# Optimization experiments

Hardware: AMD Instinct MI355X
Metric: run time of the kernel (lower is better)

## Reference

```python
import jax, jax.numpy as jnp
import numpy as np

B, T, D = 32, 4096, 256
W = 128          # window_size
EPS = 1e-5


def setup_inputs() -> dict:
    key = jax.random.key(0)
    kx, = jax.random.split(key, 1)
    x = jax.random.normal(kx, (B, T, D), dtype=jnp.float32)
    weight = jnp.ones((D,), dtype=jnp.float32)
    bias = jnp.zeros((D,), dtype=jnp.float32)
    return {"x": x, "weight": weight, "bias": bias}


def reference(x, weight, bias):
    # TemporalNorm, mode='standard', causal rolling window W, no mask, affine.
    Bs, Ts, Ds = x.shape
    idx = jnp.arange(Ts)
    l = jnp.clip(idx - W + 1, 0, None)   # left window index (inclusive)
    r = idx                               # right window index (inclusive, causal)

    # inclusive prefix sums over time, padded with a leading zero row
    sx = jnp.cumsum(x, axis=1)
    sx2 = jnp.cumsum(x * x, axis=1)

    def window_sum(cum):
        cum_pad = jnp.pad(cum, ((0, 0), (1, 0), (0, 0)))  # [B, T+1, D]
        return cum_pad[:, r + 1, :] - cum_pad[:, l, :]     # [B, T, D]

    win_sx = window_sum(sx)
    win_sx2 = window_sum(sx2)

    # mask is None -> per-window count = r - l + 1 (cumsum of ones)
    counts = (r - l + 1).astype(x.dtype)                   # [T]
    denom = jnp.maximum(counts, 1.0)[None, :, None]        # [1, T, 1]

    loc = win_sx / denom
    var = win_sx2 / denom - loc * loc
    scale = jnp.sqrt(var + EPS)

    y = (x - loc) / scale
    y = y * weight[None, None, :] + bias[None, None, :]
    return y
```

## Files before the change

kernel.cpp:

```cpp
#include <hip/hip_runtime.h>

constexpr int Bb  = 32;
constexpr int Tt  = 4096;
constexpr int Dd  = 256;
constexpr int Ww  = 128;
constexpr float EPSF = 1e-5f;

constexpr int CT  = 128;
constexpr int NC  = Tt / CT;
constexpr int TPC = Dd / 2;
constexpr int CPB = 2;
constexpr int NWG = Bb * NC / CPB;
constexpr int UF  = 8;

__global__ __launch_bounds__(256, 2)
void TemporalNorm_kernel(const float* __restrict__ x,
                         const float* __restrict__ wgt,
                         const float* __restrict__ bia,
                         float* __restrict__ out) {
    const int i  = blockIdx.x;
    const int lb = (i & 7) * (NWG / 8) + (i >> 3);
    const int b     = lb / (NC / CPB);
    const int cpair = lb % (NC / CPB);
    const int sub   = threadIdx.x / TPC;
    const int d2    = threadIdx.x % TPC;
    const int c  = cpair * CPB + sub;
    const int t0 = c * CT;

    const float2* __restrict__ xb = reinterpret_cast<const float2*>(x   + (size_t)b * Tt * Dd) + d2;
    float2*       __restrict__ ob = reinterpret_cast<float2*>      (out + (size_t)b * Tt * Dd) + d2;
    const float wx = wgt[2 * d2], wy = wgt[2 * d2 + 1];
    const float bx = bia[2 * d2], by = bia[2 * d2 + 1];
    constexpr int S = Dd / 2;

    float s1x = 0.f, s2x = 0.f, s1y = 0.f, s2y = 0.f;

    if (t0 >= Ww) {
        {
            float u1x = 0.f, u2x = 0.f, u1y = 0.f, u2y = 0.f;
            for (int t = t0 - Ww; t < t0; t += UF) {
                float2 a[UF];
#pragma unroll
                for (int j = 0; j < UF; ++j) a[j] = xb[(t + j) * S];
#pragma unroll
                for (int j = 0; j < UF; j += 2) {
                    s1x += a[j].x;  s2x += a[j].x * a[j].x;
                    s1y += a[j].y;  s2y += a[j].y * a[j].y;
                    u1x += a[j+1].x; u2x += a[j+1].x * a[j+1].x;
                    u1y += a[j+1].y; u2y += a[j+1].y * a[j+1].y;
                }
            }
            s1x += u1x; s2x += u2x; s1y += u1y; s2y += u2y;
        }

        const float rn = 1.0f / (float)Ww;
        auto step = [&](float a, float o, float& s1, float& s2, float w, float bi) -> float {
            s1 += a - o;
            s2 += a * a - o * o;
            float loc = s1 * rn;
            float var = s2 * rn - loc * loc;
            return (a - loc) * rsqrtf(var + EPSF) * w + bi;
        };

        float2 A[UF], O[UF];
#pragma unroll
        for (int j = 0; j < UF; ++j) {
            A[j] = xb[(t0 + j) * S];
            O[j] = xb[(t0 + j - Ww) * S];
        }
        int tt = t0;
        for (; tt + UF < t0 + CT; tt += UF) {
            float2 An[UF], On[UF];
#pragma unroll
            for (int j = 0; j < UF; ++j) {
                An[j] = xb[(tt + UF + j) * S];
                On[j] = xb[(tt + UF + j - Ww) * S];
            }
#pragma unroll
            for (int j = 0; j < UF; ++j) {
                float2 r;
                r.x = step(A[j].x, O[j].x, s1x, s2x, wx, bx);
                r.y = step(A[j].y, O[j].y, s1y, s2y, wy, by);
                ob[(tt + j) * S] = r;
            }
#pragma unroll
            for (int j = 0; j < UF; ++j) { A[j] = An[j]; O[j] = On[j]; }
        }
#pragma unroll
        for (int j = 0; j < UF; ++j) {
            float2 r;
            r.x = step(A[j].x, O[j].x, s1x, s2x, wx, bx);
            r.y = step(A[j].y, O[j].y, s1y, s2y, wy, by);
            ob[(tt + j) * S] = r;
        }
    } else {
        for (int t = 0; t < CT; t += 4) {
            float2 a[4];
#pragma unroll
            for (int j = 0; j < 4; ++j) a[j] = xb[(t + j) * S];
#pragma unroll
            for (int j = 0; j < 4; ++j) {
                s1x += a[j].x; s2x += a[j].x * a[j].x;
                s1y += a[j].y; s2y += a[j].y * a[j].y;
                float rnv = 1.0f / (float)(t + j + 1);
                float lx = s1x * rnv, ly = s1y * rnv;
                float vx = s2x * rnv - lx * lx;
                float vy = s2y * rnv - ly * ly;
                float2 r;
                r.x = (a[j].x - lx) * rsqrtf(vx + EPSF) * wx + bx;
                r.y = (a[j].y - ly) * rsqrtf(vy + EPSF) * wy + by;
                ob[(t + j) * S] = r;
            }
        }
    }
}

extern "C" void kernel_launch(void* const* d_in, const int* in_sizes, int n_in,
                              void* d_out, int out_size, void* d_ws, size_t ws_size,
                              hipStream_t stream) {
    const float* x   = (const float*)d_in[0];
    const float* wgt = (const float*)d_in[1];
    const float* bia = (const float*)d_in[2];
    float* out = (float*)d_out;

    hipLaunchKernelGGL(TemporalNorm_kernel, dim3(NWG), dim3(256), 0, stream,
                       x, wgt, bia, out);
}
```

Baseline: 65.98 us.

## Process two time chunks per single-wave thread with float4 loads and nontemporal stores

Restructures the kernel so each 64-thread block covers all 256 channels as float4 per thread and processes two adjacent 128-step chunks in interleaved fashion, giving more independent loads in flight per thread. Output writes become nontemporal stores, and the first chunk pair reuses the causal running sums to seed the second chunk instead of reloading a warm-up window. The block count stays the same while threads per block drop from 256 to 64, so per-CU wave count and register pressure change; fewer total waves may reduce latency hiding.

```diff
diff --git a/kernel.cpp b/kernel.cpp
--- a/kernel.cpp
+++ b/kernel.cpp
@@ -8,108 +8,117 @@
 
 constexpr int CT  = 128;
 constexpr int NC  = Tt / CT;
-constexpr int TPC = Dd / 2;
-constexpr int CPB = 2;
-constexpr int NWG = Bb * NC / CPB;
-constexpr int UF  = 8;
+constexpr int NP  = NC / 2;
+constexpr int NWG = Bb * NP;
+constexpr int S4  = Dd / 4;
 
-__global__ __launch_bounds__(256, 2)
+typedef float f32x4 __attribute__((ext_vector_type(4)));
+
+__global__ __launch_bounds__(64)
 void TemporalNorm_kernel(const float* __restrict__ x,
                          const float* __restrict__ wgt,
                          const float* __restrict__ bia,
                          float* __restrict__ out) {
     const int i  = blockIdx.x;
     const int lb = (i & 7) * (NWG / 8) + (i >> 3);
-    const int b     = lb / (NC / CPB);
-    const int cpair = lb % (NC / CPB);
-    const int sub   = threadIdx.x / TPC;
-    const int d2    = threadIdx.x % TPC;
-    const int c  = cpair * CPB + sub;
-    const int t0 = c * CT;
+    const int b  = lb / NP;
+    const int p  = lb % NP;
+    const int d4 = threadIdx.x;
+    const int t0A = (2 * p) * CT;
+    const int t0B = t0A + CT;
 
-    const float2* __restrict__ xb = reinterpret_cast<const float2*>(x   + (size_t)b * Tt * Dd) + d2;
-    float2*       __restrict__ ob = reinterpret_cast<float2*>      (out + (size_t)b * Tt * Dd) + d2;
-    const float wx = wgt[2 * d2], wy = wgt[2 * d2 + 1];
-    const float bx = bia[2 * d2], by = bia[2 * d2 + 1];
-    constexpr int S = Dd / 2;
+    const f32x4* __restrict__ xb = reinterpret_cast<const f32x4*>(x   + (size_t)b * Tt * Dd) + d4;
+    f32x4*       __restrict__ ob = reinterpret_cast<f32x4*>      (out + (size_t)b * Tt * Dd) + d4;
+    const f32x4 w4 = reinterpret_cast<const f32x4*>(wgt)[d4];
+    const f32x4 b4 = reinterpret_cast<const f32x4*>(bia)[d4];
 
-    float s1x = 0.f, s2x = 0.f, s1y = 0.f, s2y = 0.f;
+    float s1A[4] = {0,0,0,0}, s2A[4] = {0,0,0,0};
+    float s1B[4] = {0,0,0,0}, s2B[4] = {0,0,0,0};
 
-    if (t0 >= Ww) {
-        {
-            float u1x = 0.f, u2x = 0.f, u1y = 0.f, u2y = 0.f;
-            for (int t = t0 - Ww; t < t0; t += UF) {
-                float2 a[UF];
+    const float rn = 1.0f / (float)Ww;
+
+    auto acc = [&](const f32x4& a, float* s1, float* s2) {
 #pragma unroll
-                for (int j = 0; j < UF; ++j) a[j] = xb[(t + j) * S];
+        for (int k = 0; k < 4; ++k) { s1[k] += a[k]; s2[k] += a[k] * a[k]; }
+    };
+    auto step4 = [&](const f32x4& a, const f32x4& o, float* s1, float* s2) -> f32x4 {
+        f32x4 r;
 #pragma unroll
-                for (int j = 0; j < UF; j += 2) {
-                    s1x += a[j].x;  s2x += a[j].x * a[j].x;
-                    s1y += a[j].y;  s2y += a[j].y * a[j].y;
-                    u1x += a[j+1].x; u2x += a[j+1].x * a[j+1].x;
-                    u1y += a[j+1].y; u2y += a[j+1].y * a[j+1].y;
-                }
-            }
-            s1x += u1x; s2x += u2x; s1y += u1y; s2y += u2y;
+        for (int k = 0; k < 4; ++k) {
+            s1[k] += a[k] - o[k];
+            s2[k] += a[k] * a[k] - o[k] * o[k];
+            float loc = s1[k] * rn;
+            float var = s2[k] * rn - loc * loc;
+            r[k] = (a[k] - loc) * rsqrtf(var + EPSF) * w4[k] + b4[k];
         }
+        return r;
+    };
+    auto grow4 = [&](const f32x4& a, float* s1, float* s2, float n) -> f32x4 {
+        float rnv = 1.0f / n;
+        f32x4 r;
+#pragma unroll
+        for (int k = 0; k < 4; ++k) {
+            float loc = s1[k] * rnv;
+            float var = s2[k] * rnv - loc * loc;
+            r[k] = (a[k] - loc) * rsqrtf(var + EPSF) * w4[k] + b4[k];
+        }
+        return r;
+    };
 
-        const float rn = 1.0f / (float)Ww;
-        auto step = [&](float a, float o, float& s1, float& s2, float w, float bi) -> float {
-            s1 += a - o;
-            s2 += a * a - o * o;
-            float loc = s1 * rn;
-            float var = s2 * rn - loc * loc;
-            return (a - loc) * rsqrtf(var + EPSF) * w + bi;
-        };
-
-        float2 A[UF], O[UF];
+    if (p != 0) {
+        for (int t = 0; t < Ww; t += 4) {
+            f32x4 aA[4], aB[4];
 #pragma unroll
-        for (int j = 0; j < UF; ++j) {
-            A[j] = xb[(t0 + j) * S];
-            O[j] = xb[(t0 + j - Ww) * S];
+            for (int j = 0; j < 4; ++j) aA[j] = xb[(t0A - Ww + t + j) * S4];
+#pragma unroll
+            for (int j = 0; j < 4; ++j) aB[j] = xb[(t0B - Ww + t + j) * S4];
+#pragma unroll
+            for (int j = 0; j < 4; ++j) { acc(aA[j], s1A, s2A); acc(aB[j], s1B, s2B); }
         }
-        int tt = t0;
-        for (; tt + UF < t0 + CT; tt += UF) {
-            float2 An[UF], On[UF];
+        for (int t = 0; t < CT; t += 4) {
+            f32x4 aA[4], oA[4], aB[4], oB[4];
 #pragma unroll
-            for (int j = 0; j < UF; ++j) {
-                An[j] = xb[(tt + UF + j) * S];
-                On[j] = xb[(tt + UF + j - Ww) * S];
+            for (int j = 0; j < 4; ++j) aA[j] = xb[(t0A + t + j) * S4];
+#pragma unroll
+            for (int j = 0; j < 4; ++j) oA[j] = xb[(t0A + t + j - Ww) * S4];
+#pragma unroll
+            for (int j = 0; j < 4; ++j) aB[j] = xb[(t0B + t + j) * S4];
+#pragma unroll
+            for (int j = 0; j < 4; ++j) oB[j] = xb[(t0B + t + j - Ww) * S4];
+#pragma unroll
+            for (int j = 0; j < 4; ++j) {
+                f32x4 rA = step4(aA[j], oA[j], s1A, s2A);
+                __builtin_nontemporal_store(rA, &ob[(t0A + t + j) * S4]);
             }
 #pragma unroll
-            for (int j = 0; j < UF; ++j) {
-                float2 r;
-                r.x = step(A[j].x, O[j].x, s1x, s2x, wx, bx);
-                r.y = step(A[j].y, O[j].y, s1y, s2y, wy, by);
-                ob[(tt + j) * S] = r;
+            for (int j = 0; j < 4; ++j) {
+                f32x4 rB = step4(aB[j], oB[j], s1B, s2B);
+                __builtin_nontemporal_store(rB, &ob[(t0B + t + j) * S4]);
             }
-#pragma unroll
-            for (int j = 0; j < UF; ++j) { A[j] = An[j]; O[j] = On[j]; }
-        }
-#pragma unroll
-        for (int j = 0; j < UF; ++j) {
-            float2 r;
-            r.x = step(A[j].x, O[j].x, s1x, s2x, wx, bx);
-            r.y = step(A[j].y, O[j].y, s1y, s2y, wy, by);
-            ob[(tt + j) * S] = r;
         }
     } else {
         for (int t = 0; t < CT; t += 4) {
-            float2 a[4];
+            f32x4 a[4];
 #pragma unroll
-            for (int j = 0; j < 4; ++j) a[j] = xb[(t + j) * S];
+            for (int j = 0; j < 4; ++j) a[j] = xb[(t + j) * S4];
 #pragma unroll
             for (int j = 0; j < 4; ++j) {
-                s1x += a[j].x; s2x += a[j].x * a[j].x;
-                s1y += a[j].y; s2y += a[j].y * a[j].y;
-                float rnv = 1.0f / (float)(t + j + 1);
-                float lx = s1x * rnv, ly = s1y * rnv;
-                float vx = s2x * rnv - lx * lx;
-                float vy = s2y * rnv - ly * ly;
-                float2 r;
-                r.x = (a[j].x - lx) * rsqrtf(vx + EPSF) * wx + bx;
-                r.y = (a[j].y - ly) * rsqrtf(vy + EPSF) * wy + by;
-                ob[(t + j) * S] = r;
+                acc(a[j], s1A, s2A);
+                f32x4 r = grow4(a[j], s1A, s2A, (float)(t + j + 1));
+                __builtin_nontemporal_store(r, &ob[(t + j) * S4]);
+                acc(a[j], s1B, s2B);
+            }
+        }
+        for (int t = 0; t < CT; t += 4) {
+            f32x4 aB[4], oB[4];
+#pragma unroll
+            for (int j = 0; j < 4; ++j) aB[j] = xb[(t0B + t + j) * S4];
+#pragma unroll
+            for (int j = 0; j < 4; ++j) oB[j] = xb[(t0B + t + j - Ww) * S4];
+#pragma unroll
+            for (int j = 0; j < 4; ++j) {
+                f32x4 rB = step4(aB[j], oB[j], s1B, s2B);
+                __builtin_nontemporal_store(rB, &ob[(t0B + t + j) * S4]);
             }
         }
     }
@@ -123,6 +132,6 @@
     const float* bia = (const float*)d_in[2];
     float* out = (float*)d_out;
 
-    hipLaunchKernelGGL(TemporalNorm_kernel, dim3(NWG), dim3(256), 0, stream,
+    hipLaunchKernelGGL(TemporalNorm_kernel, dim3(NWG), dim3(64), 0, stream,
                        x, wgt, bia, out);
 }
```

After: 80.99 us. +22.7%, slower.

## Stage input through LDS ring buffers with async global_load_lds pipelining

Applied to the files above, without the earlier changes.

Replaces the register-prefetch sliding-window kernel with single-wavefront workgroups, each handling a 64-column slice across 256 timesteps. Input rows, both the leading and the trailing window edge, are streamed into triple- and double-buffered LDS rings using async global-to-LDS loads, with manual vmcnt/lgkmcnt waits and sched barriers to overlap loads with compute. The aim is to hide memory latency and raise memory-level parallelism. It adds hand-tuned wait counts that must match the issue order exactly, and uses narrower per-thread columns with scalar stores.

```diff
diff --git a/kernel.cpp b/kernel.cpp
--- a/kernel.cpp
+++ b/kernel.cpp
@@ -1,4 +1,5 @@
 #include <hip/hip_runtime.h>
+#include <cstdint>
 
 constexpr int Bb  = 32;
 constexpr int Tt  = 4096;
@@ -6,112 +7,149 @@
 constexpr int Ww  = 128;
 constexpr float EPSF = 1e-5f;
 
-constexpr int CT  = 128;
-constexpr int NC  = Tt / CT;
-constexpr int TPC = Dd / 2;
-constexpr int CPB = 2;
-constexpr int NWG = Bb * NC / CPB;
-constexpr int UF  = 8;
+constexpr int CT   = 256;
+constexpr int DG   = 64;
+constexpr int NDG  = Dd / DG;
+constexpr int NC   = Tt / CT;
+constexpr int NWG  = Bb * NC * NDG;
+constexpr int BATCH = 16;
+constexpr int WB   = Ww / BATCH;
+constexpr int MB   = CT / BATCH;
 
-__global__ __launch_bounds__(256, 2)
+constexpr unsigned vm_enc(unsigned vm) {
+    return (vm & 15u) | ((vm >> 4) << 14) | (7u << 4) | (15u << 8);
+}
+constexpr unsigned lgkm0_enc = 15u | (3u << 14) | (7u << 4) | (0u << 8);
+
+#define SBAR() __builtin_amdgcn_sched_barrier(0)
+#define WAITVM(n)  do { SBAR(); __builtin_amdgcn_s_waitcnt(vm_enc(n)); SBAR(); } while (0)
+#define WAITLGKM() do { SBAR(); __builtin_amdgcn_s_waitcnt(lgkm0_enc); SBAR(); } while (0)
+
+__global__ __launch_bounds__(64)
 void TemporalNorm_kernel(const float* __restrict__ x,
                          const float* __restrict__ wgt,
                          const float* __restrict__ bia,
                          float* __restrict__ out) {
+    __shared__ __align__(16) float Aring[3 * BATCH * DG];
+    __shared__ __align__(16) float Oring[2 * BATCH * DG];
+
     const int i  = blockIdx.x;
     const int lb = (i & 7) * (NWG / 8) + (i >> 3);
-    const int b     = lb / (NC / CPB);
-    const int cpair = lb % (NC / CPB);
-    const int sub   = threadIdx.x / TPC;
-    const int d2    = threadIdx.x % TPC;
-    const int c  = cpair * CPB + sub;
+    const int dg   = lb % NDG;
+    const int rest = lb / NDG;
+    const int c = rest % NC;
+    const int b = rest / NC;
     const int t0 = c * CT;
 
-    const float2* __restrict__ xb = reinterpret_cast<const float2*>(x   + (size_t)b * Tt * Dd) + d2;
-    float2*       __restrict__ ob = reinterpret_cast<float2*>      (out + (size_t)b * Tt * Dd) + d2;
-    const float wx = wgt[2 * d2], wy = wgt[2 * d2 + 1];
-    const float bx = bia[2 * d2], by = bia[2 * d2 + 1];
-    constexpr int S = Dd / 2;
+    const int lane = threadIdx.x;
+    const int lrow = lane >> 4;
+    const int lcol = (lane & 15) * 4;
 
-    float s1x = 0.f, s2x = 0.f, s1y = 0.f, s2y = 0.f;
+    const float wv = wgt[dg * DG + lane];
+    const float bv = bia[dg * DG + lane];
+    float* __restrict__ op = out + (size_t)b * Tt * Dd + dg * DG + lane;
 
-    if (t0 >= Ww) {
-        {
-            float u1x = 0.f, u2x = 0.f, u1y = 0.f, u2y = 0.f;
-            for (int t = t0 - Ww; t < t0; t += UF) {
-                float2 a[UF];
+    float s1 = 0.0f, s2 = 0.0f;
+    const float rn = 1.0f / (float)Ww;
+
+    if (c == 0) {
+        const float* xp = x + (size_t)b * Tt * Dd + dg * DG + lane;
+        for (int t = 0; t < Ww; t += 8) {
+            float a[8];
 #pragma unroll
-                for (int j = 0; j < UF; ++j) a[j] = xb[(t + j) * S];
+            for (int j = 0; j < 8; ++j) a[j] = xp[(size_t)(t + j) * Dd];
 #pragma unroll
-                for (int j = 0; j < UF; j += 2) {
-                    s1x += a[j].x;  s2x += a[j].x * a[j].x;
-                    s1y += a[j].y;  s2y += a[j].y * a[j].y;
-                    u1x += a[j+1].x; u2x += a[j+1].x * a[j+1].x;
-                    u1y += a[j+1].y; u2y += a[j+1].y * a[j+1].y;
-                }
+            for (int j = 0; j < 8; ++j) {
+                s1 += a[j]; s2 += a[j] * a[j];
+                float rnv = 1.0f / (float)(t + j + 1);
+                float loc = s1 * rnv;
+                float var = s2 * rnv - loc * loc;
+                op[(size_t)(t + j) * Dd] = (a[j] - loc) * rsqrtf(var + EPSF) * wv + bv;
             }
-            s1x += u1x; s2x += u2x; s1y += u1y; s2y += u2y;
         }
+        for (int t = Ww; t < CT; t += 8) {
+            float a[8], o[8];
+#pragma unroll
+            for (int j = 0; j < 8; ++j) a[j] = xp[(size_t)(t + j) * Dd];
+#pragma unroll
+            for (int j = 0; j < 8; ++j) o[j] = xp[(size_t)(t + j - Ww) * Dd];
+#pragma unroll
+            for (int j = 0; j < 8; ++j) {
+                s1 += a[j] - o[j];
+                s2 += (a[j] - o[j]) * (a[j] + o[j]);
+                float loc = s1 * rn;
+                float var = s2 * rn - loc * loc;
+                op[(size_t)(t + j) * Dd] = (a[j] - loc) * rsqrtf(var + EPSF) * wv + bv;
+            }
+        }
+        return;
+    }
 
-        const float rn = 1.0f / (float)Ww;
-        auto step = [&](float a, float o, float& s1, float& s2, float w, float bi) -> float {
+    auto stageA = [&](int k) {
+        const size_t rbase = (size_t)b * Tt + (t0 - Ww + BATCH * k);
+        char* lds0 = (char*)Aring + (k % 3) * 4096;
+#pragma unroll
+        for (int j = 0; j < 4; ++j) {
+            const float* g = x + (rbase + 4 * j + lrow) * Dd + dg * DG + lcol;
+            __builtin_amdgcn_global_load_lds(
+                (const __attribute__((address_space(1))) void*)g,
+                (__attribute__((address_space(3))) void*)(lds0 + j * 1024), 16, 0, 0);
+        }
+    };
+    auto stageO = [&](int k) {
+        const size_t rbase = (size_t)b * Tt + (t0 - Ww + BATCH * k);
+        char* lds0 = (char*)Oring + (k % 2) * 4096;
+#pragma unroll
+        for (int j = 0; j < 4; ++j) {
+            const float* g = x + (rbase + 4 * j + lrow) * Dd + dg * DG + lcol;
+            __builtin_amdgcn_global_load_lds(
+                (const __attribute__((address_space(1))) void*)g,
+                (__attribute__((address_space(3))) void*)(lds0 + j * 1024), 16, 0, 0);
+        }
+    };
+
+    stageA(0); stageA(1); stageA(2);
+    SBAR();
+
+    for (int w = 0; w < WB; ++w) {
+        WAITVM(8);
+        const int as_ = (w % 3) * (BATCH * DG);
+        float av[BATCH];
+#pragma unroll
+        for (int s = 0; s < BATCH; ++s) av[s] = Aring[as_ + s * DG + lane];
+#pragma unroll
+        for (int s = 0; s < BATCH; ++s) { float a = av[s]; s1 += a; s2 += a * a; }
+        WAITLGKM();
+        stageA(w + 3);
+        if (w == 6) stageO(0);
+        if (w == 7) stageO(1);
+        SBAR();
+    }
+
+    for (int m = 0; m < MB; ++m) {
+        if (m == 0)            WAITVM(8);
+        else if (m >= 14)      WAITVM(16);
+        else                   WAITVM(24);
+        const int as_ = ((8 + m) % 3) * (BATCH * DG);
+        const int os_ = (m % 2) * (BATCH * DG);
+        float av[BATCH], ov[BATCH];
+#pragma unroll
+        for (int s = 0; s < BATCH; ++s) av[s] = Aring[as_ + s * DG + lane];
+#pragma unroll
+        for (int s = 0; s < BATCH; ++s) ov[s] = Oring[os_ + s * DG + lane];
+#pragma unroll
+        for (int s = 0; s < BATCH; ++s) {
+            float a = av[s], o = ov[s];
             s1 += a - o;
-            s2 += a * a - o * o;
+            s2 += (a - o) * (a + o);
             float loc = s1 * rn;
             float var = s2 * rn - loc * loc;
-            return (a - loc) * rsqrtf(var + EPSF) * w + bi;
-        };
-
-        float2 A[UF], O[UF];
-#pragma unroll
-        for (int j = 0; j < UF; ++j) {
-            A[j] = xb[(t0 + j) * S];
-            O[j] = xb[(t0 + j - Ww) * S];
+            op[(size_t)(t0 + BATCH * m + s) * Dd] = (a - loc) * rsqrtf(var + EPSF) * wv + bv;
         }
-        int tt = t0;
-        for (; tt + UF < t0 + CT; tt += UF) {
-            float2 An[UF], On[UF];
-#pragma unroll
-            for (int j = 0; j < UF; ++j) {
-                An[j] = xb[(tt + UF + j) * S];
-                On[j] = xb[(tt + UF + j - Ww) * S];
-            }
-#pragma unroll
-            for (int j = 0; j < UF; ++j) {
-                float2 r;
-                r.x = step(A[j].x, O[j].x, s1x, s2x, wx, bx);
-                r.y = step(A[j].y, O[j].y, s1y, s2y, wy, by);
-                ob[(tt + j) * S] = r;
-            }
-#pragma unroll
-            for (int j = 0; j < UF; ++j) { A[j] = An[j]; O[j] = On[j]; }
-        }
-#pragma unroll
-        for (int j = 0; j < UF; ++j) {
-            float2 r;
-            r.x = step(A[j].x, O[j].x, s1x, s2x, wx, bx);
-            r.y = step(A[j].y, O[j].y, s1y, s2y, wy, by);
-            ob[(tt + j) * S] = r;
-        }
-    } else {
-        for (int t = 0; t < CT; t += 4) {
-            float2 a[4];
-#pragma unroll
-            for (int j = 0; j < 4; ++j) a[j] = xb[(t + j) * S];
-#pragma unroll
-            for (int j = 0; j < 4; ++j) {
-                s1x += a[j].x; s2x += a[j].x * a[j].x;
-                s1y += a[j].y; s2y += a[j].y * a[j].y;
-                float rnv = 1.0f / (float)(t + j + 1);
-                float lx = s1x * rnv, ly = s1y * rnv;
-                float vx = s2x * rnv - lx * lx;
-                float vy = s2y * rnv - ly * ly;
-                float2 r;
-                r.x = (a[j].x - lx) * rsqrtf(vx + EPSF) * wx + bx;
-                r.y = (a[j].y - ly) * rsqrtf(vy + EPSF) * wy + by;
-                ob[(t + j) * S] = r;
-            }
-        }
+        WAITLGKM();
+        if (m <= 12) stageA(11 + m);
+        if (m <= 13) stageO(2 + m);
+        SBAR();
     }
 }
 
@@ -123,6 +161,6 @@
     const float* bia = (const float*)d_in[2];
     float* out = (float*)d_out;
 
-    hipLaunchKernelGGL(TemporalNorm_kernel, dim3(NWG), dim3(256), 0, stream,
+    hipLaunchKernelGGL(TemporalNorm_kernel, dim3(NWG), dim3(64), 0, stream,
                        x, wgt, bia, out);
 }
```

After: 70.40 us. +6.7%, slower.
